# Kernel tuning notes

Hardware: AMD Instinct MI355X
Metric: run time of the kernel (lower is better)

## Reference

```python
import jax, jax.numpy as jnp
import numpy as np

K = 32            # config.k: active latents per token (batch top-k)
THRESHOLD_LR = 0.01
B, S, F = 8, 256, 16384


def setup_inputs() -> dict:
    key = jax.random.key(0)
    k1, k2 = jax.random.split(key)
    x = jax.random.normal(k1, (B, S, F), dtype=jnp.float32)
    token_mask = jax.random.randint(k2, (B, S), 0, 2, dtype=jnp.int32)
    threshold = jnp.zeros((), dtype=jnp.float32)  # persistent EMA buffer, init 0.0
    return {"x": x, "token_mask": token_mask, "threshold": threshold}


def reference(x, token_mask, threshold):
    # Training path of BatchTopKActivationFunction.forward
    b, s, f = x.shape
    num_tokens = b * s
    k_total = K * num_tokens
    neg_min = jnp.finfo(x.dtype).min
    # mask out tokens: x[~token_mask] = finfo.min (so they never enter top-k)
    xm = jnp.where(token_mask.astype(bool)[:, :, None], x, neg_min)
    flat = xm.reshape(-1)                       # [b*s*f]
    vals, idx = jax.lax.top_k(flat, k_total)    # global top-k over flattened tensor
    # scatter relu'd top-k values back into a zero tensor
    result = jnp.zeros_like(flat).at[idx].set(jax.nn.relu(vals)).reshape(b, s, f)
    # EMA threshold update: min of strictly-positive selected values
    pos = vals > 0
    min_pos = jnp.min(jnp.where(pos, vals, jnp.inf))
    new_threshold = jnp.where(
        jnp.any(pos),
        (1.0 - THRESHOLD_LR) * threshold + THRESHOLD_LR * min_pos,
        threshold,
    )
    return result, new_threshold
```

## Files before the change

kernel.cpp:

```cpp
#include <hip/hip_runtime.h>

#define N_ELEMS  33554432
#define N4       8388608
#define N_TOKENS 2048
#define F4       4096
#define K_TOTAL  65536u
#define NBINS    4096

#define C_NG       4096
#define C_WINTH    4097
#define C_CANDTH   4098
#define C_NEED     4099
#define C_FB       4100
#define C_N2       4101
#define N_CTR_END  4160

#define GLIST_OFF  8192u
#define CAPG       4194304u
#define LIST2_OFF  (GLIST_OFF + 2u*CAPG)
#define CAP2       4096u
#define FB1_OFF    16777216u
#define CAPF       2097152u
#define FB2_OFF    (FB1_OFF + 2u*CAPF)

__device__ __forceinline__ unsigned keyOf(float f) {
    unsigned b = __float_as_uint(f);
    return b ^ ((unsigned)((int)b >> 31) | 0x80000000u);
}
__device__ __forceinline__ float valOf(unsigned u) {
    unsigned b = (u & 0x80000000u) ? (u ^ 0x80000000u) : ~u;
    return __uint_as_float(b);
}
__device__ __forceinline__ unsigned umaxu(unsigned a, unsigned b) { return a > b ? a : b; }

__global__ void k_init(unsigned* __restrict__ ws) {
    int t = blockIdx.x * 256 + threadIdx.x;
    if (t < N_CTR_END) ws[t] = 0u;
}

#define GBUF 1024
__global__ __launch_bounds__(512) void k_hist(const float4* __restrict__ x,
                                              const int* __restrict__ mask,
                                              unsigned* __restrict__ ws,
                                              float4* __restrict__ out) {
    __shared__ unsigned lh[NBINS];
    __shared__ uint2 sbuf[GBUF];
    __shared__ unsigned s_cnt, s_base;
    const int tok = blockIdx.x;
    float4* ot = out + (size_t)tok * F4;
    const float4 z = make_float4(0.f, 0.f, 0.f, 0.f);
    if (!mask[tok]) {
        for (int j = threadIdx.x; j < F4; j += 512) ot[j] = z;
        return;
    }
    for (int b = threadIdx.x; b < NBINS; b += 512) lh[b] = 0u;
    if (threadIdx.x == 0) s_cnt = 0u;
    __syncthreads();
    uint2* glist = (uint2*)(ws + GLIST_OFF);
    const float4* xt = x + (size_t)tok * F4;
    const unsigned baseIdx = (unsigned)tok * 16384u;
    for (int j = threadIdx.x; j < F4; j += 512) {
        float4 v = xt[j];
        ot[j] = z;
        float fv[4] = {v.x, v.y, v.z, v.w};
        #pragma unroll
        for (int c = 0; c < 4; c++) {
            float f = fv[c];
            if (f >= 2.0f) {
                unsigned u = keyOf(f);
                unsigned bin = (u - 0xC0000000u) >> 12;
                if (bin > 4095u) bin = 4095u;
                atomicAdd(&lh[bin], 1u);
                unsigned slot = atomicAdd(&s_cnt, 1u);
                uint2 e = make_uint2(u, baseIdx + (unsigned)j * 4u + (unsigned)c);
                if (slot < GBUF) sbuf[slot] = e;
                else { unsigned g = atomicAdd(&ws[C_NG], 1u); if (g < CAPG) glist[g] = e; }
            }
        }
    }
    __syncthreads();
    for (int b = threadIdx.x; b < NBINS; b += 512) {
        unsigned c = lh[b];
        if (c) atomicAdd(&ws[b], c);
    }
    unsigned cnt = s_cnt; if (cnt > GBUF) cnt = GBUF;
    if (threadIdx.x == 0) s_base = atomicAdd(&ws[C_NG], cnt);
    __syncthreads();
    for (unsigned j = threadIdx.x; j < cnt; j += 512) {
        unsigned p = s_base + j;
        if (p < CAPG) glist[p] = sbuf[j];
    }
}

__global__ __launch_bounds__(1024) void k_scan1(unsigned* __restrict__ ws) {
    __shared__ unsigned sc[1024];
    __shared__ unsigned sB1, sKA, sFound;
    const int t = threadIdx.x;
    unsigned vv[4];
    unsigned s = 0u;
    #pragma unroll
    for (int j = 0; j < 4; ++j) { vv[j] = ws[t * 4 + j]; s += vv[j]; }
    if (t == 0) sFound = 0u;
    sc[t] = s;
    __syncthreads();
    for (int off = 1; off < 1024; off <<= 1) {
        unsigned a = sc[t];
        unsigned b = (t + off < 1024) ? sc[t + off] : 0u;
        __syncthreads();
        sc[t] = a + b;
        __syncthreads();
    }
    unsigned run = (t < 1023) ? sc[t + 1] : 0u;
    #pragma unroll
    for (int j = 3; j >= 0; --j) {
        unsigned prev = run; run += vv[j];
        if (run >= K_TOTAL && prev < K_TOTAL) {
            sB1 = (unsigned)(t * 4 + j); sKA = prev; sFound = 1u;
        }
    }
    __syncthreads();
    if (t == 0) {
        unsigned total = sc[0];
        unsigned ng = ws[C_NG];
        unsigned fb = (sFound == 0u) || (total < K_TOTAL) || (sB1 == 4095u) || (ng > CAPG);
        ws[C_FB] = fb ? 1u : 0u;
        if (!fb) {
            unsigned candTh = 0xC0000000u + (sB1 << 12);
            ws[C_CANDTH] = candTh;
            ws[C_WINTH]  = candTh + 0x1000u;
            ws[C_NEED]   = K_TOTAL - sKA;
        }
    }
}

__global__ __launch_bounds__(256) void k_scatter(unsigned* __restrict__ ws,
                                                 float* __restrict__ out) {
    if (ws[C_FB]) return;
    const unsigned winTh = ws[C_WINTH], candTh = ws[C_CANDTH];
    unsigned ng = ws[C_NG]; if (ng > CAPG) ng = CAPG;
    uint2* glist = (uint2*)(ws + GLIST_OFF);
    uint2* list2 = (uint2*)(ws + LIST2_OFF);
    const unsigned stride = gridDim.x * 256;
    for (unsigned i = blockIdx.x * 256 + threadIdx.x; i < ng; i += stride) {
        uint2 e = glist[i];
        if (e.x >= winTh) out[e.y] = valOf(e.x);
        else if (e.x >= candTh) {
            unsigned g = atomicAdd(&ws[C_N2], 1u);
            if (g < CAP2) list2[g] = e;
        }
    }
}

__global__ __launch_bounds__(256) void k_tail(unsigned* __restrict__ ws,
                                              float* __restrict__ out,
                                              const float* __restrict__ thr) {
    if (ws[C_FB]) return;
    __shared__ uint2 ent[CAP2];
    __shared__ unsigned sred[256];
    const int t = threadIdx.x;
    unsigned rawn2 = ws[C_N2];
    if (rawn2 > CAP2) { if (t == 0) ws[C_FB] = 1u; return; }
    const unsigned n2 = rawn2;
    const unsigned need = ws[C_NEED];
    uint2* list2 = (uint2*)(ws + LIST2_OFF);
    for (unsigned i = t; i < n2; i += 256) ent[i] = list2[i];
    __syncthreads();
    unsigned minSel = 0xFFFFFFFFu;
    for (unsigned i = t; i < n2; i += 256) {
        uint2 e = ent[i];
        unsigned rank = 0u;
        for (unsigned j = 0; j < n2; ++j) {
            uint2 o = ent[j];
            rank += (o.x > e.x || (o.x == e.x && o.y < e.y)) ? 1u : 0u;
        }
        if (rank < need) {
            out[e.y] = valOf(e.x);
            if (e.x < minSel) minSel = e.x;
        }
    }
    sred[t] = minSel;
    __syncthreads();
    for (int off = 128; off > 0; off >>= 1) {
        if (t < off) sred[t] = sred[t] < sred[t + off] ? sred[t] : sred[t + off];
        __syncthreads();
    }
    if (t == 0) {
        out[N_ELEMS] = 0.99f * thr[0] + 0.01f * valOf(sred[0]);
    }
}

__global__ __launch_bounds__(1024) void k_fallback(const float4* __restrict__ x,
                                                   const int* __restrict__ mask,
                                                   unsigned* __restrict__ ws,
                                                   float* __restrict__ out,
                                                   const float* __restrict__ thr) {
    if (ws[C_FB] == 0u) return;
    __shared__ unsigned lh[NBINS];
    __shared__ unsigned sred[1024];
    __shared__ unsigned sB1, sKA, sMode, sNegmin, sB2, sNeed, sCnt;
    const int t = threadIdx.x;
    for (int b = t; b < NBINS; b += 1024) lh[b] = 0u;
    __syncthreads();
    unsigned negmin = 0u;
    for (int tok = 0; tok < N_TOKENS; ++tok) {
        if (!mask[tok]) continue;
        const float4* xt = x + (size_t)tok * F4;
        for (int j = t; j < F4; j += 1024) {
            float4 v = xt[j];
            float fv[4] = {v.x, v.y, v.z, v.w};
            #pragma unroll
            for (int c = 0; c < 4; ++c) {
                float f = fv[c];
                unsigned u = keyOf(f);
                atomicAdd(&lh[u >> 20], 1u);
                if (f > 0.0f) negmin = umaxu(negmin, ~u);
            }
        }
    }
    __syncthreads();
    sred[t] = negmin; __syncthreads();
    for (int off = 512; off > 0; off >>= 1) {
        if (t < off) sred[t] = umaxu(sred[t], sred[t + off]);
        __syncthreads();
    }
    if (t == 0) {
        sNegmin = sred[0];
        unsigned tot = 0u;
        for (int b = 0; b < NBINS; ++b) tot += lh[b];
        if (tot <= K_TOTAL) sMode = 1u;
        else {
            sMode = 0u;
            unsigned run = 0u, prev = 0u; int b1 = 0;
            for (int b = NBINS - 1; b >= 0; --b) {
                prev = run; run += lh[b];
                if (run >= K_TOTAL && prev < K_TOTAL) { b1 = b; break; }
            }
            sB1 = (unsigned)b1; sKA = prev;
        }
        sCnt = 0u;
    }
    __syncthreads();
    if (sMode == 1u) {
        for (int tok = 0; tok < N_TOKENS; ++tok) {
            if (!mask[tok]) continue;
            const float4* xt = x + (size_t)tok * F4;
            float* ot = out + (size_t)tok * 16384;
            for (int j = t; j < F4; j += 1024) {
                float4 v = xt[j];
                ot[j * 4 + 0] = fmaxf(v.x, 0.f); ot[j * 4 + 1] = fmaxf(v.y, 0.f);
                ot[j * 4 + 2] = fmaxf(v.z, 0.f); ot[j * 4 + 3] = fmaxf(v.w, 0.f);
            }
        }
        if (t == 0) {
            float th = thr[0], newt = th;
            if (sNegmin) newt = 0.99f * th + 0.01f * valOf(~sNegmin);
            out[N_ELEMS] = newt;
        }
        return;
    }
    const unsigned B1c = sB1;
    uint2* fb1 = (uint2*)(ws + FB1_OFF);
    for (int tok = 0; tok < N_TOKENS; ++tok) {
        if (!mask[tok]) continue;
        const float4* xt = x + (size_t)tok * F4;
        const unsigned baseIdx = (unsigned)tok * 16384u;
        for (int j = t; j < F4; j += 1024) {
            float4 v = xt[j];
            float fv[4] = {v.x, v.y, v.z, v.w};
            #pragma unroll
            for (int c = 0; c < 4; ++c) {
                float f = fv[c];
                unsigned u = keyOf(f);
                unsigned p = u >> 20;
                unsigned idx = baseIdx + (unsigned)j * 4u + (unsigned)c;
                if (p > B1c) out[idx] = fmaxf(f, 0.f);
                else if (p == B1c) {
                    unsigned g = atomicAdd(&sCnt, 1u);
                    if (g < CAPF) fb1[g] = make_uint2(u, idx);
                }
            }
        }
    }
    __syncthreads();
    unsigned n1 = sCnt > CAPF ? CAPF : sCnt;
    __syncthreads();
    if (t < 256) lh[t] = 0u;
    if (t == 0) sCnt = 0u;
    __syncthreads();
    for (unsigned i = t; i < n1; i += 1024)
        atomicAdd(&lh[(fb1[i].x >> 12) & 255u], 1u);
    __syncthreads();
    if (t == 0) {
        unsigned run = sKA, prev = sKA; int b2 = 0;
        for (int b = 255; b >= 0; --b) {
            prev = run; run += lh[b];
            if (run >= K_TOTAL) { b2 = b; break; }
        }
        sB2 = (unsigned)b2; sNeed = K_TOTAL - prev;
    }
    __syncthreads();
    const unsigned B2 = sB2, need = sNeed;
    uint2* fb2 = (uint2*)(ws + FB2_OFF);
    for (unsigned i = t; i < n1; i += 1024) {
        uint2 e = fb1[i];
        unsigned bb = (e.x >> 12) & 255u;
        if (bb > B2) out[e.y] = fmaxf(valOf(e.x), 0.f);
        else if (bb == B2) {
            unsigned g = atomicAdd(&sCnt, 1u);
            if (g < CAPF) fb2[g] = e;
        }
    }
    __syncthreads();
    unsigned n2 = sCnt > CAPF ? CAPF : sCnt;
    unsigned minSel = 0xFFFFFFFFu;
    for (unsigned i = t; i < n2; i += 1024) {
        uint2 e = fb2[i];
        unsigned rank = 0u;
        for (unsigned jj = 0; jj < n2; ++jj) {
            uint2 o = fb2[jj];
            rank += (o.x > e.x || (o.x == e.x && o.y < e.y)) ? 1u : 0u;
        }
        if (rank < need) { out[e.y] = fmaxf(valOf(e.x), 0.f); if (e.x < minSel) minSel = e.x; }
    }
    __syncthreads();
    sred[t] = minSel; __syncthreads();
    for (int off = 512; off > 0; off >>= 1) {
        if (t < off) sred[t] = sred[t] < sred[t + off] ? sred[t] : sred[t + off];
        __syncthreads();
    }
    if (t == 0) {
        float th = thr[0], newt = th;
        unsigned vku = sred[0];
        if (vku != 0xFFFFFFFFu) {
            float vk = valOf(vku);
            float minpos; int any;
            if (vk > 0.f) { minpos = vk; any = 1; }
            else { any = (sNegmin != 0u); minpos = any ? valOf(~sNegmin) : 0.f; }
            if (any) newt = 0.99f * th + 0.01f * minpos;
        }
        out[N_ELEMS] = newt;
    }
}

extern "C" void kernel_launch(void* const* d_in, const int* in_sizes, int n_in,
                              void* d_out, int out_size, void* d_ws, size_t ws_size,
                              hipStream_t stream) {
    const float4* x  = (const float4*)d_in[0];
    const int* mask  = (const int*)d_in[1];
    const float* thr = (const float*)d_in[2];
    float* out       = (float*)d_out;
    unsigned* ws     = (unsigned*)d_ws;

    k_init    <<<17, 256, 0, stream>>>(ws);
    k_hist    <<<N_TOKENS, 512, 0, stream>>>(x, mask, ws, (float4*)out);
    k_scan1   <<<1, 1024, 0, stream>>>(ws);
    k_scatter <<<256, 256, 0, stream>>>(ws, out);
    k_tail    <<<1, 256, 0, stream>>>(ws, out, thr);
    k_fallback<<<1, 1024, 0, stream>>>(x, mask, ws, out, thr);
}
```

Measured before the change: 271.2 us.

## Fuse histogram, scan, scatter and tail into one persistent kernel with grid barriers

Replaces four separate launches (histogram, scan, scatter, tail) with one persistent kernel sized to occupancy. Blocks loop over tokens and accumulate a per-block shared histogram flushed once at the end, and software grid barriers built on global atomics separate the phases. The scan drops to 256 threads with 16 bins each. The aim is to remove launch gaps and most of the global histogram atomics. The cost is that correctness depends on every block being co-resident, and per-block histogram flushes plus spin barriers add their own overhead.

```diff
diff --git a/kernel.cpp b/kernel.cpp
--- a/kernel.cpp
+++ b/kernel.cpp
@@ -13,6 +13,9 @@
 #define C_NEED     4099
 #define C_FB       4100
 #define C_N2       4101
+#define C_BAR0     4104
+#define C_BAR1     4105
+#define C_BAR2     4106
 #define N_CTR_END  4160
 
 #define GLIST_OFF  8192u
@@ -23,6 +26,8 @@
 #define CAPF       2097152u
 #define FB2_OFF    (FB1_OFF + 2u*CAPF)
 
+#define GBUF 1024
+
 __device__ __forceinline__ unsigned keyOf(float f) {
     unsigned b = __float_as_uint(f);
     return b ^ ((unsigned)((int)b >> 31) | 0x80000000u);
@@ -33,140 +38,156 @@
 }
 __device__ __forceinline__ unsigned umaxu(unsigned a, unsigned b) { return a > b ? a : b; }
 
+__device__ __forceinline__ void gbar(unsigned* __restrict__ slot, unsigned nb) {
+    __syncthreads();
+    if (threadIdx.x == 0) {
+        __threadfence();
+        atomicAdd(slot, 1u);
+        while (__hip_atomic_load(slot, __ATOMIC_RELAXED, __HIP_MEMORY_SCOPE_AGENT) < nb) {
+            __builtin_amdgcn_s_sleep(2);
+        }
+        __threadfence();
+    }
+    __syncthreads();
+}
+
 __global__ void k_init(unsigned* __restrict__ ws) {
     int t = blockIdx.x * 256 + threadIdx.x;
     if (t < N_CTR_END) ws[t] = 0u;
 }
 
-#define GBUF 1024
-__global__ __launch_bounds__(512) void k_hist(const float4* __restrict__ x,
-                                              const int* __restrict__ mask,
-                                              unsigned* __restrict__ ws,
-                                              float4* __restrict__ out) {
-    __shared__ unsigned lh[NBINS];
-    __shared__ uint2 sbuf[GBUF];
-    __shared__ unsigned s_cnt, s_base;
-    const int tok = blockIdx.x;
-    float4* ot = out + (size_t)tok * F4;
+__global__ __launch_bounds__(256, 4) void k_fused(const float4* __restrict__ x,
+                                                  const int* __restrict__ mask,
+                                                  const float* __restrict__ thr,
+                                                  unsigned* __restrict__ ws,
+                                                  float* __restrict__ out) {
+    __shared__ __align__(16) unsigned smem[8448];
+    __shared__ unsigned s_cnt, s_base, s_b1, s_ka, s_found;
+    const int tid = threadIdx.x;
+    const unsigned nb = gridDim.x;
+    const unsigned gtid = blockIdx.x * 256u + (unsigned)tid;
+    const unsigned gstride = nb * 256u;
+
+    unsigned* lh = smem;
+    uint2* sbuf = (uint2*)(smem + NBINS);
+    for (int b = tid; b < NBINS; b += 256) lh[b] = 0u;
+    uint2* glist = (uint2*)(ws + GLIST_OFF);
     const float4 z = make_float4(0.f, 0.f, 0.f, 0.f);
-    if (!mask[tok]) {
-        for (int j = threadIdx.x; j < F4; j += 512) ot[j] = z;
-        return;
-    }
-    for (int b = threadIdx.x; b < NBINS; b += 512) lh[b] = 0u;
-    if (threadIdx.x == 0) s_cnt = 0u;
-    __syncthreads();
-    uint2* glist = (uint2*)(ws + GLIST_OFF);
-    const float4* xt = x + (size_t)tok * F4;
-    const unsigned baseIdx = (unsigned)tok * 16384u;
-    for (int j = threadIdx.x; j < F4; j += 512) {
-        float4 v = xt[j];
-        ot[j] = z;
-        float fv[4] = {v.x, v.y, v.z, v.w};
-        #pragma unroll
-        for (int c = 0; c < 4; c++) {
-            float f = fv[c];
-            if (f >= 2.0f) {
-                unsigned u = keyOf(f);
-                unsigned bin = (u - 0xC0000000u) >> 12;
-                if (bin > 4095u) bin = 4095u;
-                atomicAdd(&lh[bin], 1u);
-                unsigned slot = atomicAdd(&s_cnt, 1u);
-                uint2 e = make_uint2(u, baseIdx + (unsigned)j * 4u + (unsigned)c);
-                if (slot < GBUF) sbuf[slot] = e;
-                else { unsigned g = atomicAdd(&ws[C_NG], 1u); if (g < CAPG) glist[g] = e; }
-            }
-        }
-    }
-    __syncthreads();
-    for (int b = threadIdx.x; b < NBINS; b += 512) {
+    for (unsigned tok = blockIdx.x; tok < N_TOKENS; tok += nb) {
+        float4* ot = (float4*)out + (size_t)tok * F4;
+        if (!mask[tok]) {
+            for (int j = tid; j < F4; j += 256) ot[j] = z;
+            continue;
+        }
+        if (tid == 0) s_cnt = 0u;
+        __syncthreads();
+        const float4* xt = x + (size_t)tok * F4;
+        const unsigned baseIdx = (unsigned)tok * 16384u;
+        for (int j = tid; j < F4; j += 512) {
+            float4 v0 = xt[j];
+            float4 v1 = xt[j + 256];
+            ot[j] = z; ot[j + 256] = z;
+            float fv[8] = {v0.x, v0.y, v0.z, v0.w, v1.x, v1.y, v1.z, v1.w};
+            #pragma unroll
+            for (int c = 0; c < 8; ++c) {
+                float f = fv[c];
+                if (f >= 2.0f) {
+                    unsigned u = keyOf(f);
+                    unsigned bin = (u - 0xC0000000u) >> 12;
+                    if (bin > 4095u) bin = 4095u;
+                    atomicAdd(&lh[bin], 1u);
+                    unsigned slot = atomicAdd(&s_cnt, 1u);
+                    unsigned idx = baseIdx + ((unsigned)(c < 4 ? j : j + 256)) * 4u + (unsigned)(c & 3);
+                    uint2 e = make_uint2(u, idx);
+                    if (slot < GBUF) sbuf[slot] = e;
+                    else { unsigned g = atomicAdd(&ws[C_NG], 1u); if (g < CAPG) glist[g] = e; }
+                }
+            }
+        }
+        __syncthreads();
+        unsigned cnt = s_cnt; if (cnt > GBUF) cnt = GBUF;
+        if (tid == 0) s_base = atomicAdd(&ws[C_NG], cnt);
+        __syncthreads();
+        for (unsigned j2 = (unsigned)tid; j2 < cnt; j2 += 256u) {
+            unsigned p = s_base + j2;
+            if (p < CAPG) glist[p] = sbuf[j2];
+        }
+        __syncthreads();
+    }
+    __syncthreads();
+    for (int b = tid; b < NBINS; b += 256) {
         unsigned c = lh[b];
         if (c) atomicAdd(&ws[b], c);
     }
-    unsigned cnt = s_cnt; if (cnt > GBUF) cnt = GBUF;
-    if (threadIdx.x == 0) s_base = atomicAdd(&ws[C_NG], cnt);
-    __syncthreads();
-    for (unsigned j = threadIdx.x; j < cnt; j += 512) {
-        unsigned p = s_base + j;
-        if (p < CAPG) glist[p] = sbuf[j];
-    }
-}
-
-__global__ __launch_bounds__(1024) void k_scan1(unsigned* __restrict__ ws) {
-    __shared__ unsigned sc[1024];
-    __shared__ unsigned sB1, sKA, sFound;
-    const int t = threadIdx.x;
-    unsigned vv[4];
-    unsigned s = 0u;
-    #pragma unroll
-    for (int j = 0; j < 4; ++j) { vv[j] = ws[t * 4 + j]; s += vv[j]; }
-    if (t == 0) sFound = 0u;
-    sc[t] = s;
-    __syncthreads();
-    for (int off = 1; off < 1024; off <<= 1) {
-        unsigned a = sc[t];
-        unsigned b = (t + off < 1024) ? sc[t + off] : 0u;
-        __syncthreads();
-        sc[t] = a + b;
-        __syncthreads();
-    }
-    unsigned run = (t < 1023) ? sc[t + 1] : 0u;
-    #pragma unroll
-    for (int j = 3; j >= 0; --j) {
-        unsigned prev = run; run += vv[j];
-        if (run >= K_TOTAL && prev < K_TOTAL) {
-            sB1 = (unsigned)(t * 4 + j); sKA = prev; sFound = 1u;
-        }
-    }
-    __syncthreads();
-    if (t == 0) {
-        unsigned total = sc[0];
-        unsigned ng = ws[C_NG];
-        unsigned fb = (sFound == 0u) || (total < K_TOTAL) || (sB1 == 4095u) || (ng > CAPG);
-        ws[C_FB] = fb ? 1u : 0u;
-        if (!fb) {
-            unsigned candTh = 0xC0000000u + (sB1 << 12);
-            ws[C_CANDTH] = candTh;
-            ws[C_WINTH]  = candTh + 0x1000u;
-            ws[C_NEED]   = K_TOTAL - sKA;
-        }
-    }
-}
-
-__global__ __launch_bounds__(256) void k_scatter(unsigned* __restrict__ ws,
-                                                 float* __restrict__ out) {
+    gbar(&ws[C_BAR0], nb);
+
+    if (blockIdx.x == 0) {
+        unsigned* sc = smem;
+        unsigned vv[16]; unsigned ssum = 0u;
+        #pragma unroll
+        for (int j = 0; j < 16; ++j) { vv[j] = ws[tid * 16 + j]; ssum += vv[j]; }
+        if (tid == 0) s_found = 0u;
+        sc[tid] = ssum;
+        __syncthreads();
+        for (int off = 1; off < 256; off <<= 1) {
+            unsigned a = sc[tid];
+            unsigned b2 = (tid + off < 256) ? sc[tid + off] : 0u;
+            __syncthreads();
+            sc[tid] = a + b2;
+            __syncthreads();
+        }
+        unsigned run = (tid < 255) ? sc[tid + 1] : 0u;
+        #pragma unroll
+        for (int j = 15; j >= 0; --j) {
+            unsigned prev = run; run += vv[j];
+            if (run >= K_TOTAL && prev < K_TOTAL) {
+                s_b1 = (unsigned)(tid * 16 + j); s_ka = prev; s_found = 1u;
+            }
+        }
+        __syncthreads();
+        if (tid == 0) {
+            unsigned total = sc[0];
+            unsigned ng = ws[C_NG];
+            unsigned fb = (s_found == 0u) || (total < K_TOTAL) || (s_b1 == 4095u) || (ng > CAPG);
+            ws[C_FB] = fb ? 1u : 0u;
+            if (!fb) {
+                unsigned candTh = 0xC0000000u + (s_b1 << 12);
+                ws[C_CANDTH] = candTh;
+                ws[C_WINTH]  = candTh + 0x1000u;
+                ws[C_NEED]   = K_TOTAL - s_ka;
+            }
+        }
+    }
+    gbar(&ws[C_BAR1], nb);
+
+    if (!ws[C_FB]) {
+        const unsigned winTh = ws[C_WINTH], candTh = ws[C_CANDTH];
+        unsigned ng = ws[C_NG]; if (ng > CAPG) ng = CAPG;
+        uint2* list2 = (uint2*)(ws + LIST2_OFF);
+        for (unsigned i = gtid; i < ng; i += gstride) {
+            uint2 e = glist[i];
+            if (e.x >= winTh) out[e.y] = valOf(e.x);
+            else if (e.x >= candTh) {
+                unsigned g = atomicAdd(&ws[C_N2], 1u);
+                if (g < CAP2) list2[g] = e;
+            }
+        }
+    }
+    gbar(&ws[C_BAR2], nb);
+
+    if (blockIdx.x != 0) return;
     if (ws[C_FB]) return;
-    const unsigned winTh = ws[C_WINTH], candTh = ws[C_CANDTH];
-    unsigned ng = ws[C_NG]; if (ng > CAPG) ng = CAPG;
-    uint2* glist = (uint2*)(ws + GLIST_OFF);
-    uint2* list2 = (uint2*)(ws + LIST2_OFF);
-    const unsigned stride = gridDim.x * 256;
-    for (unsigned i = blockIdx.x * 256 + threadIdx.x; i < ng; i += stride) {
-        uint2 e = glist[i];
-        if (e.x >= winTh) out[e.y] = valOf(e.x);
-        else if (e.x >= candTh) {
-            unsigned g = atomicAdd(&ws[C_N2], 1u);
-            if (g < CAP2) list2[g] = e;
-        }
-    }
-}
-
-__global__ __launch_bounds__(256) void k_tail(unsigned* __restrict__ ws,
-                                              float* __restrict__ out,
-                                              const float* __restrict__ thr) {
-    if (ws[C_FB]) return;
-    __shared__ uint2 ent[CAP2];
-    __shared__ unsigned sred[256];
-    const int t = threadIdx.x;
     unsigned rawn2 = ws[C_N2];
-    if (rawn2 > CAP2) { if (t == 0) ws[C_FB] = 1u; return; }
+    if (rawn2 > CAP2) { if (tid == 0) ws[C_FB] = 1u; return; }
+    uint2* ent = (uint2*)smem;
+    unsigned* red = smem + 2u * CAP2;
     const unsigned n2 = rawn2;
     const unsigned need = ws[C_NEED];
     uint2* list2 = (uint2*)(ws + LIST2_OFF);
-    for (unsigned i = t; i < n2; i += 256) ent[i] = list2[i];
+    for (unsigned i = (unsigned)tid; i < n2; i += 256u) ent[i] = list2[i];
     __syncthreads();
     unsigned minSel = 0xFFFFFFFFu;
-    for (unsigned i = t; i < n2; i += 256) {
+    for (unsigned i = (unsigned)tid; i < n2; i += 256u) {
         uint2 e = ent[i];
         unsigned rank = 0u;
         for (unsigned j = 0; j < n2; ++j) {
@@ -178,14 +199,14 @@
             if (e.x < minSel) minSel = e.x;
         }
     }
-    sred[t] = minSel;
+    red[tid] = minSel;
     __syncthreads();
     for (int off = 128; off > 0; off >>= 1) {
-        if (t < off) sred[t] = sred[t] < sred[t + off] ? sred[t] : sred[t + off];
-        __syncthreads();
-    }
-    if (t == 0) {
-        out[N_ELEMS] = 0.99f * thr[0] + 0.01f * valOf(sred[0]);
+        if (tid < off) red[tid] = red[tid] < red[tid + off] ? red[tid] : red[tid + off];
+        __syncthreads();
+    }
+    if (tid == 0) {
+        out[N_ELEMS] = 0.99f * thr[0] + 0.01f * valOf(red[0]);
     }
 }
 
@@ -351,10 +372,26 @@
     float* out       = (float*)d_out;
     unsigned* ws     = (unsigned*)d_ws;
 
+    static int grid_blocks = 0;
+    if (grid_blocks == 0) {
+        int occ = 0;
+        if (hipOccupancyMaxActiveBlocksPerMultiprocessor(&occ, k_fused, 256, 0) != hipSuccess || occ < 1)
+            occ = 1;
+        if (occ > 4) occ = 4;
+        int ncu = 256;
+        int dev = 0;
+        hipDeviceProp_t prop;
+        if (hipGetDevice(&dev) == hipSuccess &&
+            hipGetDeviceProperties(&prop, dev) == hipSuccess &&
+            prop.multiProcessorCount > 0)
+            ncu = prop.multiProcessorCount;
+        long g = (long)occ * (long)ncu;
+        if (g > 1024) g = 1024;
+        if (g < 1) g = 1;
+        grid_blocks = (int)g;
+    }
+
     k_init    <<<17, 256, 0, stream>>>(ws);
-    k_hist    <<<N_TOKENS, 512, 0, stream>>>(x, mask, ws, (float4*)out);
-    k_scan1   <<<1, 1024, 0, stream>>>(ws);
-    k_scatter <<<256, 256, 0, stream>>>(ws, out);
-    k_tail    <<<1, 256, 0, stream>>>(ws, out, thr);
+    k_fused   <<<grid_blocks, 256, 0, stream>>>(x, mask, thr, ws, out);
     k_fallback<<<1, 1024, 0, stream>>>(x, mask, ws, out, thr);
 }
```

Measured after the change: 656.3 us. 2.42x slower.

## Fuse scan into scatter and tail, merge fallback, unroll histogram loads

Applied to the files above, without the earlier changes.

Drops the separate single-block scan kernel. Every scatter block now redoes the 4096-bin prefix scan itself, and the tail kernel repeats the scan to decide between the fast path and the fallback, which is merged into the same 1024-thread kernel. This cuts the launch count from six to four. The histogram kernel issues four float4 loads per thread before processing them, giving more memory-level parallelism, and the scatter grid doubles. The cost is redundant scan work in every scatter block.

```diff
diff --git a/kernel.cpp b/kernel.cpp
--- a/kernel.cpp
+++ b/kernel.cpp
@@ -8,10 +8,6 @@
 #define NBINS    4096
 
 #define C_NG       4096
-#define C_WINTH    4097
-#define C_CANDTH   4098
-#define C_NEED     4099
-#define C_FB       4100
 #define C_N2       4101
 #define N_CTR_END  4160
 
@@ -23,6 +19,8 @@
 #define CAPF       2097152u
 #define FB2_OFF    (FB1_OFF + 2u*CAPF)
 
+#define GBUF 1024
+
 __device__ __forceinline__ unsigned keyOf(float f) {
     unsigned b = __float_as_uint(f);
     return b ^ ((unsigned)((int)b >> 31) | 0x80000000u);
@@ -38,7 +36,6 @@
     if (t < N_CTR_END) ws[t] = 0u;
 }
 
-#define GBUF 1024
 __global__ __launch_bounds__(512) void k_hist(const float4* __restrict__ x,
                                               const int* __restrict__ mask,
                                               unsigned* __restrict__ ws,
@@ -47,24 +44,31 @@
     __shared__ uint2 sbuf[GBUF];
     __shared__ unsigned s_cnt, s_base;
     const int tok = blockIdx.x;
+    const int tid = threadIdx.x;
     float4* ot = out + (size_t)tok * F4;
     const float4 z = make_float4(0.f, 0.f, 0.f, 0.f);
     if (!mask[tok]) {
-        for (int j = threadIdx.x; j < F4; j += 512) ot[j] = z;
+        for (int j = tid; j < F4; j += 512) ot[j] = z;
         return;
     }
-    for (int b = threadIdx.x; b < NBINS; b += 512) lh[b] = 0u;
-    if (threadIdx.x == 0) s_cnt = 0u;
+    for (int b = tid; b < NBINS; b += 512) lh[b] = 0u;
+    if (tid == 0) s_cnt = 0u;
     __syncthreads();
     uint2* glist = (uint2*)(ws + GLIST_OFF);
     const float4* xt = x + (size_t)tok * F4;
     const unsigned baseIdx = (unsigned)tok * 16384u;
-    for (int j = threadIdx.x; j < F4; j += 512) {
-        float4 v = xt[j];
-        ot[j] = z;
-        float fv[4] = {v.x, v.y, v.z, v.w};
+    #pragma unroll
+    for (int half = 0; half < 2; ++half) {
+        const int j0 = tid + half * 2048;
+        float4 v0 = xt[j0];
+        float4 v1 = xt[j0 + 512];
+        float4 v2 = xt[j0 + 1024];
+        float4 v3 = xt[j0 + 1536];
+        ot[j0] = z; ot[j0 + 512] = z; ot[j0 + 1024] = z; ot[j0 + 1536] = z;
+        float fv[16] = {v0.x, v0.y, v0.z, v0.w, v1.x, v1.y, v1.z, v1.w,
+                        v2.x, v2.y, v2.z, v2.w, v3.x, v3.y, v3.z, v3.w};
         #pragma unroll
-        for (int c = 0; c < 4; c++) {
+        for (int c = 0; c < 16; ++c) {
             float f = fv[c];
             if (f >= 2.0f) {
                 unsigned u = keyOf(f);
@@ -72,76 +76,66 @@
                 if (bin > 4095u) bin = 4095u;
                 atomicAdd(&lh[bin], 1u);
                 unsigned slot = atomicAdd(&s_cnt, 1u);
-                uint2 e = make_uint2(u, baseIdx + (unsigned)j * 4u + (unsigned)c);
+                unsigned j = (unsigned)(j0 + (c >> 2) * 512);
+                uint2 e = make_uint2(u, baseIdx + j * 4u + (unsigned)(c & 3));
                 if (slot < GBUF) sbuf[slot] = e;
                 else { unsigned g = atomicAdd(&ws[C_NG], 1u); if (g < CAPG) glist[g] = e; }
             }
         }
     }
     __syncthreads();
-    for (int b = threadIdx.x; b < NBINS; b += 512) {
+    for (int b = tid; b < NBINS; b += 512) {
         unsigned c = lh[b];
         if (c) atomicAdd(&ws[b], c);
     }
     unsigned cnt = s_cnt; if (cnt > GBUF) cnt = GBUF;
-    if (threadIdx.x == 0) s_base = atomicAdd(&ws[C_NG], cnt);
-    __syncthreads();
-    for (unsigned j = threadIdx.x; j < cnt; j += 512) {
+    if (tid == 0) s_base = atomicAdd(&ws[C_NG], cnt);
+    __syncthreads();
+    for (unsigned j = tid; j < cnt; j += 512) {
         unsigned p = s_base + j;
         if (p < CAPG) glist[p] = sbuf[j];
     }
 }
 
-__global__ __launch_bounds__(1024) void k_scan1(unsigned* __restrict__ ws) {
-    __shared__ unsigned sc[1024];
-    __shared__ unsigned sB1, sKA, sFound;
+__global__ __launch_bounds__(256) void k_scatter(unsigned* __restrict__ ws,
+                                                 float* __restrict__ out) {
+    __shared__ unsigned sc[256];
+    __shared__ unsigned s_b1, s_ka, s_found;
     const int t = threadIdx.x;
-    unsigned vv[4];
+    unsigned vv[16];
     unsigned s = 0u;
     #pragma unroll
-    for (int j = 0; j < 4; ++j) { vv[j] = ws[t * 4 + j]; s += vv[j]; }
-    if (t == 0) sFound = 0u;
+    for (int j = 0; j < 16; ++j) { vv[j] = ws[t * 16 + j]; s += vv[j]; }
+    if (t == 0) { s_found = 0u; s_b1 = 0u; s_ka = 0u; }
     sc[t] = s;
     __syncthreads();
-    for (int off = 1; off < 1024; off <<= 1) {
+    for (int off = 1; off < 256; off <<= 1) {
         unsigned a = sc[t];
-        unsigned b = (t + off < 1024) ? sc[t + off] : 0u;
+        unsigned b = (t + off < 256) ? sc[t + off] : 0u;
         __syncthreads();
         sc[t] = a + b;
         __syncthreads();
     }
-    unsigned run = (t < 1023) ? sc[t + 1] : 0u;
+    unsigned run = (t < 255) ? sc[t + 1] : 0u;
     #pragma unroll
-    for (int j = 3; j >= 0; --j) {
+    for (int j = 15; j >= 0; --j) {
         unsigned prev = run; run += vv[j];
         if (run >= K_TOTAL && prev < K_TOTAL) {
-            sB1 = (unsigned)(t * 4 + j); sKA = prev; sFound = 1u;
-        }
-    }
-    __syncthreads();
-    if (t == 0) {
-        unsigned total = sc[0];
-        unsigned ng = ws[C_NG];
-        unsigned fb = (sFound == 0u) || (total < K_TOTAL) || (sB1 == 4095u) || (ng > CAPG);
-        ws[C_FB] = fb ? 1u : 0u;
-        if (!fb) {
-            unsigned candTh = 0xC0000000u + (sB1 << 12);
-            ws[C_CANDTH] = candTh;
-            ws[C_WINTH]  = candTh + 0x1000u;
-            ws[C_NEED]   = K_TOTAL - sKA;
-        }
-    }
-}
-
-__global__ __launch_bounds__(256) void k_scatter(unsigned* __restrict__ ws,
-                                                 float* __restrict__ out) {
-    if (ws[C_FB]) return;
-    const unsigned winTh = ws[C_WINTH], candTh = ws[C_CANDTH];
-    unsigned ng = ws[C_NG]; if (ng > CAPG) ng = CAPG;
+            s_b1 = (unsigned)(t * 16 + j); s_ka = prev; s_found = 1u;
+        }
+    }
+    __syncthreads();
+    const unsigned total = sc[0];
+    unsigned ngRaw = ws[C_NG];
+    if ((s_found == 0u) || (total < K_TOTAL) || (s_b1 == 4095u) || (ngRaw > CAPG))
+        return;
+    const unsigned candTh = 0xC0000000u + (s_b1 << 12);
+    const unsigned winTh  = candTh + 0x1000u;
+    unsigned ng = ngRaw;
     uint2* glist = (uint2*)(ws + GLIST_OFF);
     uint2* list2 = (uint2*)(ws + LIST2_OFF);
-    const unsigned stride = gridDim.x * 256;
-    for (unsigned i = blockIdx.x * 256 + threadIdx.x; i < ng; i += stride) {
+    const unsigned stride = gridDim.x * 256u;
+    for (unsigned i = blockIdx.x * 256u + (unsigned)t; i < ng; i += stride) {
         uint2 e = glist[i];
         if (e.x >= winTh) out[e.y] = valOf(e.x);
         else if (e.x >= candTh) {
@@ -151,55 +145,89 @@
     }
 }
 
-__global__ __launch_bounds__(256) void k_tail(unsigned* __restrict__ ws,
-                                              float* __restrict__ out,
-                                              const float* __restrict__ thr) {
-    if (ws[C_FB]) return;
-    __shared__ uint2 ent[CAP2];
-    __shared__ unsigned sred[256];
-    const int t = threadIdx.x;
-    unsigned rawn2 = ws[C_N2];
-    if (rawn2 > CAP2) { if (t == 0) ws[C_FB] = 1u; return; }
-    const unsigned n2 = rawn2;
-    const unsigned need = ws[C_NEED];
-    uint2* list2 = (uint2*)(ws + LIST2_OFF);
-    for (unsigned i = t; i < n2; i += 256) ent[i] = list2[i];
-    __syncthreads();
-    unsigned minSel = 0xFFFFFFFFu;
-    for (unsigned i = t; i < n2; i += 256) {
-        uint2 e = ent[i];
-        unsigned rank = 0u;
-        for (unsigned j = 0; j < n2; ++j) {
-            uint2 o = ent[j];
-            rank += (o.x > e.x || (o.x == e.x && o.y < e.y)) ? 1u : 0u;
-        }
-        if (rank < need) {
-            out[e.y] = valOf(e.x);
-            if (e.x < minSel) minSel = e.x;
-        }
-    }
-    sred[t] = minSel;
-    __syncthreads();
-    for (int off = 128; off > 0; off >>= 1) {
-        if (t < off) sred[t] = sred[t] < sred[t + off] ? sred[t] : sred[t + off];
-        __syncthreads();
-    }
-    if (t == 0) {
-        out[N_ELEMS] = 0.99f * thr[0] + 0.01f * valOf(sred[0]);
-    }
-}
-
-__global__ __launch_bounds__(1024) void k_fallback(const float4* __restrict__ x,
-                                                   const int* __restrict__ mask,
-                                                   unsigned* __restrict__ ws,
-                                                   float* __restrict__ out,
-                                                   const float* __restrict__ thr) {
-    if (ws[C_FB] == 0u) return;
-    __shared__ unsigned lh[NBINS];
-    __shared__ unsigned sred[1024];
+__global__ __launch_bounds__(1024) void k_tail(const float4* __restrict__ x,
+                                               const int* __restrict__ mask,
+                                               unsigned* __restrict__ ws,
+                                               float* __restrict__ out,
+                                               const float* __restrict__ thr) {
+    __shared__ __align__(16) unsigned smem[9216];
+    __shared__ unsigned s_b1, s_ka, s_found, s_fb, s_need, s_n2;
     __shared__ unsigned sB1, sKA, sMode, sNegmin, sB2, sNeed, sCnt;
     const int t = threadIdx.x;
+
+    {
+        unsigned* sc = smem;
+        unsigned vv[4];
+        unsigned s = 0u;
+        #pragma unroll
+        for (int j = 0; j < 4; ++j) { vv[j] = ws[t * 4 + j]; s += vv[j]; }
+        if (t == 0) { s_found = 0u; s_b1 = 0u; s_ka = 0u; }
+        sc[t] = s;
+        __syncthreads();
+        for (int off = 1; off < 1024; off <<= 1) {
+            unsigned a = sc[t];
+            unsigned b = (t + off < 1024) ? sc[t + off] : 0u;
+            __syncthreads();
+            sc[t] = a + b;
+            __syncthreads();
+        }
+        unsigned run = (t < 1023) ? sc[t + 1] : 0u;
+        #pragma unroll
+        for (int j = 3; j >= 0; --j) {
+            unsigned prev = run; run += vv[j];
+            if (run >= K_TOTAL && prev < K_TOTAL) {
+                s_b1 = (unsigned)(t * 4 + j); s_ka = prev; s_found = 1u;
+            }
+        }
+        __syncthreads();
+        if (t == 0) {
+            unsigned total = sc[0];
+            unsigned ng = ws[C_NG];
+            unsigned n2v = ws[C_N2];
+            unsigned fb = (s_found == 0u) || (total < K_TOTAL) || (s_b1 == 4095u) ||
+                          (ng > CAPG) || (n2v > CAP2);
+            s_fb = fb; s_need = K_TOTAL - s_ka; s_n2 = n2v;
+        }
+        __syncthreads();
+    }
+
+    if (!s_fb) {
+        uint2* ent = (uint2*)smem;
+        unsigned* red = smem + 8192;
+        const unsigned n2 = s_n2;
+        const unsigned need = s_need;
+        uint2* list2 = (uint2*)(ws + LIST2_OFF);
+        for (unsigned i = (unsigned)t; i < n2; i += 1024u) ent[i] = list2[i];
+        __syncthreads();
+        unsigned minSel = 0xFFFFFFFFu;
+        for (unsigned i = (unsigned)t; i < n2; i += 1024u) {
+            uint2 e = ent[i];
+            unsigned rank = 0u;
+            for (unsigned j = 0; j < n2; ++j) {
+                uint2 o = ent[j];
+                rank += (o.x > e.x || (o.x == e.x && o.y < e.y)) ? 1u : 0u;
+            }
+            if (rank < need) {
+                out[e.y] = valOf(e.x);
+                if (e.x < minSel) minSel = e.x;
+            }
+        }
+        red[t] = minSel;
+        __syncthreads();
+        for (int off = 512; off > 0; off >>= 1) {
+            if (t < off) red[t] = red[t] < red[t + off] ? red[t] : red[t + off];
+            __syncthreads();
+        }
+        if (t == 0) {
+            out[N_ELEMS] = 0.99f * thr[0] + 0.01f * valOf(red[0]);
+        }
+        return;
+    }
+
+    unsigned* lh = smem;
+    unsigned* sred = smem + 4096;
     for (int b = t; b < NBINS; b += 1024) lh[b] = 0u;
+    if (t == 0) sCnt = 0u;
     __syncthreads();
     unsigned negmin = 0u;
     for (int tok = 0; tok < N_TOKENS; ++tok) {
@@ -353,8 +381,6 @@
 
     k_init    <<<17, 256, 0, stream>>>(ws);
     k_hist    <<<N_TOKENS, 512, 0, stream>>>(x, mask, ws, (float4*)out);
-    k_scan1   <<<1, 1024, 0, stream>>>(ws);
-    k_scatter <<<256, 256, 0, stream>>>(ws, out);
-    k_tail    <<<1, 256, 0, stream>>>(ws, out, thr);
-    k_fallback<<<1, 1024, 0, stream>>>(x, mask, ws, out, thr);
-}
+    k_scatter <<<512, 256, 0, stream>>>(ws, out);
+    k_tail    <<<1, 1024, 0, stream>>>(x, mask, ws, out, thr);
+}
```

Result: no change. 267.0 us (-1.5%).
